# Kernel optimization log

Measured on AMD Instinct MI355X. Metric: run time of the kernel, lower is better.

## Reference

```python
import jax, jax.numpy as jnp
import numpy as np
import math

B, C, L, E, N = 16, 256, 2048, 512, 64
H = 2 * C  # S4 model dimension


def setup_inputs() -> dict:
    key = jax.random.key(0)
    ks = jax.random.split(key, 12)
    inp = {
        "x": jax.random.normal(ks[0], (B, C, L), dtype=jnp.float32),
        "diffusion_emb": jax.random.normal(ks[1], (B, E), dtype=jnp.float32),
        "dp_W": jax.random.normal(ks[2], (C, E), dtype=jnp.float32) / np.sqrt(E).astype(np.float32),
        "dp_b": jnp.zeros((C,), dtype=jnp.float32),
        "in_W": jax.random.normal(ks[3], (H, C), dtype=jnp.float32) / np.sqrt(C).astype(np.float32),
        "in_b": jnp.zeros((H,), dtype=jnp.float32),
        "out_W": jax.random.normal(ks[4], (2 * C, C), dtype=jnp.float32) / np.sqrt(C).astype(np.float32),
        "out_b": jnp.zeros((2 * C,), dtype=jnp.float32),
        "ln1_g": jnp.ones((H,), dtype=jnp.float32),
        "ln1_b": jnp.zeros((H,), dtype=jnp.float32),
        "ln2_g": jnp.ones((H,), dtype=jnp.float32),
        "ln2_b": jnp.zeros((H,), dtype=jnp.float32),
    }
    for i, pre in enumerate(["s41_", "s42_"]):
        k = jax.random.fold_in(key, 100 + i)
        k1, k2, k3, k4, k5 = jax.random.split(k, 5)
        # dt log-uniform in [1e-3, 1e-1] (standard S4 init)
        inp[pre + "log_dt"] = (jax.random.uniform(k1, (H,)) * (math.log(0.1) - math.log(0.001)) + math.log(0.001)).astype(jnp.float32)
        inp[pre + "A_re"] = (-0.5 * jnp.ones((H, N))).astype(jnp.float32)
        inp[pre + "A_im"] = jnp.tile(math.pi * jnp.arange(N, dtype=jnp.float32), (H, 1))
        inp[pre + "C_re"] = jax.random.normal(k2, (H, N), dtype=jnp.float32) * (0.5 ** 0.5)
        inp[pre + "C_im"] = jax.random.normal(k3, (H, N), dtype=jnp.float32) * (0.5 ** 0.5)
        inp[pre + "D"] = jax.random.normal(k4, (H,), dtype=jnp.float32)
        inp[pre + "oW"] = jax.random.normal(k5, (2 * H, H), dtype=jnp.float32) / np.sqrt(H).astype(np.float32)
        inp[pre + "ob"] = jnp.zeros((2 * H,), dtype=jnp.float32)
    return inp


def _s4(u, log_dt, A_re, A_im, C_re, C_im, D, oW, ob):
    # u: [B, H, L]. Diagonal SSM (S4D, ZOH discretization) -> FFT conv -> D skip -> GELU -> GLU output linear.
    Lq = u.shape[-1]
    dt = jnp.exp(log_dt)                       # [H]
    A = A_re + 1j * A_im                       # [H, N] diagonal state matrix
    Cc = C_re + 1j * C_im                      # [H, N]
    dtA = dt[:, None] * A                      # [H, N]
    Ct = Cc * (jnp.exp(dtA) - 1.0) / A         # ZOH-discretized C*B (B = 1)
    lr = jnp.arange(Lq)
    # Vandermonde kernel: K[h, l] = 2 Re sum_n Ct[h, n] exp(dtA[h, n] * l)
    K = 2.0 * jnp.real(jnp.einsum("hn,hnl->hl", Ct, jnp.exp(dtA[:, :, None] * lr)))  # [H, L]
    nfft = 2 * Lq
    y = jnp.fft.irfft(jnp.fft.rfft(u, n=nfft) * jnp.fft.rfft(K, n=nfft), n=nfft)[..., :Lq]
    y = y + D[None, :, None] * u
    y = jax.nn.gelu(y)
    y = jnp.einsum("oh,bhl->bol", oW, y) + ob[None, :, None]  # [B, 2H, L]
    a, b = jnp.split(y, 2, axis=1)             # GLU over channel dim
    return a * jax.nn.sigmoid(b)               # [B, H, L]


def _ln(y, g, b):
    # LayerNorm over the channel dim (module rearranges b c l -> b l c, LN(C), back)
    mu = jnp.mean(y, axis=1, keepdims=True)
    var = jnp.var(y, axis=1, keepdims=True)
    return (y - mu) * jax.lax.rsqrt(var + 1e-5) * g[None, :, None] + b[None, :, None]


def reference(x, diffusion_emb, dp_W, dp_b, in_W, in_b, out_W, out_b,
              ln1_g, ln1_b, ln2_g, ln2_b,
              s41_log_dt, s41_A_re, s41_A_im, s41_C_re, s41_C_im, s41_D, s41_oW, s41_ob,
              s42_log_dt, s42_A_re, s42_A_im, s42_C_re, s42_C_im, s42_D, s42_oW, s42_ob):
    d = diffusion_emb @ dp_W.T + dp_b          # [B, C] -> broadcast as [B, C, 1]
    y = x + d[:, :, None]
    y = jnp.einsum("oc,bcl->bol", in_W, y) + in_b[None, :, None]   # 1x1 conv: [B, 2C, L]
    y = _s4(y, s41_log_dt, s41_A_re, s41_A_im, s41_C_re, s41_C_im, s41_D, s41_oW, s41_ob)
    y = _ln(y, ln1_g, ln1_b)
    y = _s4(y, s42_log_dt, s42_A_re, s42_A_im, s42_C_re, s42_C_im, s42_D, s42_oW, s42_ob)
    y = _ln(y, ln2_g, ln2_b)
    gate, filt = jnp.split(y, 2, axis=1)
    y = jax.nn.sigmoid(gate) * jnp.tanh(filt)  # [B, C, L]
    y = jnp.einsum("oc,bcl->bol", out_W, y) + out_b[None, :, None]  # [B, 2C, L]
    residual, skip = jnp.split(y, 2, axis=1)
    return ((x + residual) / math.sqrt(2.0), skip)
```

## Files before the change

### kernel.cpp

```cpp
#include <hip/hip_runtime.h>
#include <math.h>

#define Bsz 16
#define Cch 256
#define Lsq 2048
#define Emb 512
#define Nst 64
#define Hch 512
#define KGP 2240

typedef _Float16 f16;
typedef _Float16 f16x8 __attribute__((ext_vector_type(8)));
typedef _Float16 f16x4 __attribute__((ext_vector_type(4)));
typedef float f32x4 __attribute__((ext_vector_type(4)));
typedef uint32_t u32x4 __attribute__((ext_vector_type(4)));

__device__ __forceinline__ float sigmoidf_(float x) { return 1.0f/(1.0f + __expf(-x)); }
__device__ __forceinline__ float gelu_tanh(float y) {
  float z = 0.7978845608028654f*(y + 0.044715f*y*y*y);
  return 0.5f*y*(1.0f + tanhf(z));
}

__device__ __forceinline__ void gload_lds16(const f16* g, f16* l) {
  __builtin_amdgcn_global_load_lds(
      (const __attribute__((address_space(1))) void*)g,
      (__attribute__((address_space(3))) void*)l, 16, 0, 0);
}


__global__ void k_emb(const float* __restrict__ emb, const float* __restrict__ dpW,
                      const float* __restrict__ dpb, float* __restrict__ d) {
  int b = blockIdx.x, c = threadIdx.x;
  const float* e = emb + b*Emb;
  const float* w = dpW + c*Emb;
  float s = dpb[c];
  for (int k = 0; k < Emb; ++k) s += e[k]*w[k];
  d[b*Cch + c] = s;
}

__global__ void k_f2h(const float* __restrict__ src, f16* __restrict__ dst, int n) {
  int i = blockIdx.x*256 + threadIdx.x;
  if (i < n) dst[i] = (f16)src[i];
}

__global__ void k_addemb(const float* __restrict__ x, const float* __restrict__ d,
                         f16* __restrict__ xd) {
  int i = blockIdx.x*256 + threadIdx.x;
  const float4* x4 = (const float4*)x;
  float4 v = x4[i];
  int bc = (i*4)/Lsq;
  float dd = d[bc];
  f16x4 o;
  o[0] = (f16)(v.x+dd); o[1] = (f16)(v.y+dd); o[2] = (f16)(v.z+dd); o[3] = (f16)(v.w+dd);
  ((f16x4*)xd)[i] = o;
}

__global__ void k_s4prep(const float* __restrict__ log_dt,
                         const float* __restrict__ A_re, const float* __restrict__ A_im,
                         const float* __restrict__ C_re, const float* __restrict__ C_im,
                         float* __restrict__ w_re, float* __restrict__ w_im,
                         float* __restrict__ ccr, float* __restrict__ cci) {
  int i = blockIdx.x*256 + threadIdx.x;
  if (i >= Hch*Nst) return;
  int h = i >> 6;
  float dt = expf(log_dt[h]);
  float Ar = A_re[i], Ai = A_im[i];
  float er = expf(dt*Ar);
  float wr = er*cosf(dt*Ai), wi = er*sinf(dt*Ai);
  float mag = Ar*Ar + Ai*Ai;
  float nr = wr - 1.0f, ni = wi;
  float qr = (nr*Ar + ni*Ai)/mag, qi = (ni*Ar - nr*Ai)/mag;
  float cr = C_re[i], ci = C_im[i];
  float tr = cr*qr - ci*qi, ti = cr*qi + ci*qr;
  w_re[i] = wr; w_im[i] = wi; ccr[i] = 2.0f*tr; cci[i] = -2.0f*ti;
}

__global__ __launch_bounds__(256) void k_kgen(
    const float* __restrict__ w_re, const float* __restrict__ w_im,
    const float* __restrict__ ccr, const float* __restrict__ cci,
    const float* __restrict__ Dvec,
    f16* __restrict__ Ke, f16* __restrict__ Ko) {
  __shared__ float2 wbt[64][65];
  __shared__ float2 wat[32][66];
  __shared__ float2 ccs[64];
  __shared__ float Kf[2048];
  int h = blockIdx.x, tid = threadIdx.x;
  if (tid < 64) {
    int n = tid;
    double wr = (double)w_re[h*64+n], wi = (double)w_im[h*64+n];
    double br = 1.0, bi = 0.0;
    for (int j = 0; j < 64; ++j) {
      wbt[n][j] = make_float2((float)br, (float)bi);
      double t = br*wr - bi*wi; bi = br*wi + bi*wr; br = t;
    }
    double ar = 1.0, ai = 0.0;
    for (int a = 0; a < 32; ++a) {
      wat[a][n] = make_float2((float)ar, (float)ai);
      double t = ar*br - ai*bi; ai = ar*bi + ai*br; ar = t;
    }
    ccs[n] = make_float2(ccr[h*64+n], cci[h*64+n]);
  }
  __syncthreads();
  int lane = tid & 63, wv = tid >> 6;
  float acc[8] = {0.f,0.f,0.f,0.f,0.f,0.f,0.f,0.f};
  for (int n = 0; n < 64; ++n) {
    float2 wb = wbt[n][lane];
    float2 cc = ccs[n];
    float tr = fmaf(cc.y, wb.y,  cc.x*wb.x);
    float ti = fmaf(cc.y, wb.x, -cc.x*wb.y);
    #pragma unroll
    for (int li = 0; li < 8; ++li) {
      float2 wa = wat[wv + 4*li][n];
      acc[li] = fmaf(wa.x, tr, acc[li]);
      acc[li] = fmaf(wa.y, ti, acc[li]);
    }
  }
  #pragma unroll
  for (int li = 0; li < 8; ++li)
    Kf[(wv + 4*li)*64 + lane] = acc[li];
  __syncthreads();
  if (tid == 0) Kf[0] += Dvec[h];
  __syncthreads();
  f16* keh = Ke + (size_t)h*KGP;
  f16* koh = Ko + (size_t)h*KGP;
  for (int q = tid; q < KGP; q += 256) {
    float e = (q < 2048) ? Kf[2047 - q] : 0.f;
    float o = (q < 2047) ? Kf[2046 - q] : 0.f;
    keh[q] = (f16)e; koh[q] = (f16)o;
  }
}

__device__ __forceinline__ f16x8 ldfrag(const f16* __restrict__ ke,
                                        const f16* __restrict__ ko, int q) {
  const f16* p = (q & 1) ? (ko + (q - 1)) : (ke + q);
  union { uint32_t u[4]; f16x8 v; } r;
  const uint32_t* pu = (const uint32_t*)p;
  r.u[0] = pu[0]; r.u[1] = pu[1]; r.u[2] = pu[2]; r.u[3] = pu[3];
  return r.v;
}

__global__ __launch_bounds__(256) void k_conv(
    const f16* __restrict__ u, const f16* __restrict__ Ke, const f16* __restrict__ Ko,
    f16* __restrict__ g) {
  __shared__ __align__(16) f16 Ul[16*2048];
  int h = blockIdx.x, tid = threadIdx.x;
  {
    int b = tid >> 4, pr = tid & 15;
    const f16* src = u + ((size_t)b*Hch + h)*Lsq;
    f16* dst = &Ul[b*2048];
    #pragma unroll
    for (int c = 0; c < 16; ++c) {
      int gs = c*16 + pr;
      *(f16x8*)&dst[(gs ^ b)*8] = *(const f16x8*)(src + gs*8);
    }
  }
  __syncthreads();
  int wv = tid >> 6, lane = tid & 63;
  int m = lane & 15, qd = lane >> 4;
  const f16* keh = Ke + (size_t)h*KGP;
  const f16* koh = Ko + (size_t)h*KGP;
  f16* gb = g + ((size_t)m*Hch + h)*Lsq;
  const f16* ulb = &Ul[m*2048];
  for (int pass = 0; pass < 4; ++pass) {
    int P = pass*4 + ((wv + pass) & 3);
    int i0 = P*128;
    int qb0 = 2047 - i0 - m + qd*8;
    f32x4 acc[8];
    #pragma unroll
    for (int t = 0; t < 8; ++t) acc[t] = (f32x4){0.f,0.f,0.f,0.f};
    f16x8 W[8];
    #pragma unroll
    for (int t = 0; t < 8; ++t) W[t] = ldfrag(keh, koh, qb0 - 16*t);
    int steps = 4*(P+1);
    for (int s4i = 0; s4i < steps; s4i += 4) {
      #pragma unroll
      for (int ph = 0; ph < 4; ++ph) {
        int s = s4i + ph;
        f16x8 bf = *(const f16x8*)&ulb[((4*s + qd) ^ m)*8];
        f16x8 nf0 = ldfrag(keh, koh, qb0 + 32*(s+1));
        f16x8 nf1 = ldfrag(keh, koh, qb0 - 16 + 32*(s+1));
        #pragma unroll
        for (int t = 0; t < 8; ++t)
          acc[t] = __builtin_amdgcn_mfma_f32_16x16x32_f16(W[(t - 2*ph) & 7], bf, acc[t], 0, 0, 0);
        W[(6 - 2*ph) & 7] = nf0;
        W[(7 - 2*ph) & 7] = nf1;
      }
    }
    #pragma unroll
    for (int t = 0; t < 8; ++t) {
      f16x4 o;
      #pragma unroll
      for (int r = 0; r < 4; ++r) o[r] = (f16)gelu_tanh(acc[t][r]);
      *(f16x4*)&gb[i0 + 16*t + qd*4] = o;
    }
  }
}

template<int KD, int MODE>
__global__ __launch_bounds__(256) void k_gemm(
    const f16* __restrict__ W, const f16* __restrict__ Bact,
    const float* __restrict__ bias, const float* __restrict__ xres,
    float* __restrict__ outF, f16* __restrict__ outH) {
  constexpr int TOFF = (MODE == 1) ? 512 : 256;
  __shared__ __align__(16) f16 As[2*128*64];
  __shared__ __align__(16) uint32_t Bs[32*132];
  int tid = threadIdx.x;
  int wv = tid >> 6, lane = tid & 63;
  int nt = blockIdx.x;
  int mt = blockIdx.y;
  int bb = nt >> 4;
  int l0 = (nt & 15)*128;
  int m0 = mt*128;
  int wm = (wv & 1)*64, wn = (wv >> 1)*64;
  int qd = lane >> 4, ln16 = lane & 15;

  f32x4 acc[2][4][4];
  #pragma unroll
  for (int t = 0; t < 2; ++t)
    for (int i = 0; i < 4; ++i)
      for (int j = 0; j < 4; ++j)
        acc[t][i][j] = (f32x4){0.f,0.f,0.f,0.f};

  const f16* Bbase = Bact + (size_t)bb*KD*Lsq + l0;
  int q16 = tid >> 4, nch = tid & 15;

  for (int kk = 0; kk < KD; kk += 64) {
    #pragma unroll
    for (int i = 0; i < 8; ++i) {
      int gbase = (wv*8 + i)*64;
      int G = gbase + lane;
      int t = G >> 10;
      int row = (G >> 3) & 127;
      int gsw = (G & 7) ^ (row & 7);
      const f16* src = W + (size_t)(m0 + row + t*TOFF)*KD + kk + gsw*8;
      gload_lds16(src, &As[gbase*8]);
    }
    #pragma unroll
    for (int c = 0; c < 2; ++c) {
      const f16* b0 = Bbase + (size_t)(kk + 2*q16 + 32*c)*Lsq + nch*8;
      f16x8 r0 = *(const f16x8*)b0;
      f16x8 r1 = *(const f16x8*)(b0 + Lsq);
      union { uint32_t w[8]; u32x4 v[2]; } pk;
      #pragma unroll
      for (int e = 0; e < 8; ++e) {
        union { f16 h2[2]; uint32_t u; } t2;
        t2.h2[0] = r0[e]; t2.h2[1] = r1[e];
        pk.w[e] = t2.u;
      }
      *(u32x4*)&Bs[(q16 + 16*c)*132 + nch*8]     = pk.v[0];
      *(u32x4*)&Bs[(q16 + 16*c)*132 + nch*8 + 4] = pk.v[1];
    }
    __syncthreads();
    #pragma unroll
    for (int s = 0; s < 2; ++s) {
      f16x8 afr[2][4];
      #pragma unroll
      for (int i = 0; i < 4; ++i)
        for (int t = 0; t < 2; ++t) {
          int row = wm + i*16 + ln16;
          int gp = (s*4 + qd) ^ (ln16 & 7);
          afr[t][i] = *(const f16x8*)&As[((t*128 + row)*8 + gp)*8];
        }
      f16x8 bfr[4];
      int bw0 = (s*16 + qd*4)*132 + wn + ln16;
      #pragma unroll
      for (int j = 0; j < 4; ++j) {
        union { uint32_t w2[4]; f16x8 v; } bu;
        #pragma unroll
        for (int r2 = 0; r2 < 4; ++r2) bu.w2[r2] = Bs[bw0 + j*16 + r2*132];
        bfr[j] = bu.v;
      }
      #pragma unroll
      for (int j = 0; j < 4; ++j)
        for (int i = 0; i < 4; ++i)
          for (int t = 0; t < 2; ++t)
            acc[t][i][j] = __builtin_amdgcn_mfma_f32_16x16x32_f16(afr[t][i], bfr[j], acc[t][i][j], 0, 0, 0);
    }
    __syncthreads();
  }

  #pragma unroll
  for (int i = 0; i < 4; ++i)
    for (int j = 0; j < 4; ++j)
      for (int r = 0; r < 4; ++r) {
        int ml = wm + i*16 + qd*4 + r;
        int nl = wn + j*16 + ln16;
        int mg = m0 + ml;
        int l  = l0 + nl;
        if (MODE == 0) {
          outH[((size_t)bb*Hch + mg)*Lsq + l]       = (f16)(acc[0][i][j][r] + bias[mg]);
          outH[((size_t)bb*Hch + mg + 256)*Lsq + l] = (f16)(acc[1][i][j][r] + bias[mg + 256]);
        } else if (MODE == 1) {
          float va = acc[0][i][j][r] + bias[mg];
          float vb = acc[1][i][j][r] + bias[512 + mg];
          outH[((size_t)bb*Hch + mg)*Lsq + l] = (f16)(va * sigmoidf_(vb));
        } else {
          size_t idx = ((size_t)bb*Cch + mg)*Lsq + l;
          float v0 = acc[0][i][j][r] + bias[mg];
          outF[idx] = (v0 + xres[idx]) * 0.7071067811865476f;
          float v1 = acc[1][i][j][r] + bias[mg + 256];
          outF[(size_t)Bsz*Cch*Lsq + idx] = v1;
        }
      }
}

template<int MODE>
__global__ __launch_bounds__(256) void k_ln(const f16* __restrict__ v,
                                            const float* __restrict__ gam, const float* __restrict__ bet,
                                            float* __restrict__ outF, f16* __restrict__ outH) {
  __shared__ float red[2][4][64];
  int b = blockIdx.x >> 5;
  int l = (blockIdx.x & 31)*64 + (threadIdx.x & 63);
  int wv = threadIdx.x >> 6, lane = threadIdx.x & 63;
  const f16* base = v + (size_t)b*Hch*Lsq + l;
  float s = 0.f, s2 = 0.f;
  for (int h = wv*128; h < wv*128 + 128; ++h) {
    float xv = (float)base[(size_t)h*Lsq];
    s += xv; s2 += xv*xv;
  }
  red[0][wv][lane] = s; red[1][wv][lane] = s2;
  __syncthreads();
  s  = red[0][0][lane] + red[0][1][lane] + red[0][2][lane] + red[0][3][lane];
  s2 = red[1][0][lane] + red[1][1][lane] + red[1][2][lane] + red[1][3][lane];
  float mu = s*(1.0f/Hch);
  float var = s2*(1.0f/Hch) - mu*mu;
  float rs = rsqrtf(var + 1e-5f);
  if (MODE == 0) {
    f16* ob = outH + (size_t)b*Hch*Lsq + l;
    for (int h = wv*128; h < wv*128 + 128; ++h)
      ob[(size_t)h*Lsq] = (f16)(((float)base[(size_t)h*Lsq] - mu)*rs*gam[h] + bet[h]);
  } else {
    f16* ob = outH + (size_t)b*Cch*Lsq + l;
    for (int c = wv*64; c < wv*64 + 64; ++c) {
      float xg = ((float)base[(size_t)c*Lsq] - mu)*rs*gam[c] + bet[c];
      float xf = ((float)base[(size_t)(c+Cch)*Lsq] - mu)*rs*gam[c+Cch] + bet[c+Cch];
      float xfc = fminf(fmaxf(xf, -15.f), 15.f);
      float e = __expf(2.f*xfc);
      ob[(size_t)c*Lsq] = (f16)(sigmoidf_(xg) * ((e-1.f)/(e+1.f)));
    }
  }
}

extern "C" void kernel_launch(void* const* d_in, const int* in_sizes, int n_in,
                              void* d_out, int out_size, void* d_ws, size_t ws_size,
                              hipStream_t stream) {
  const float* x    = (const float*)d_in[0];
  const float* emb  = (const float*)d_in[1];
  const float* dpW  = (const float*)d_in[2];
  const float* dpb  = (const float*)d_in[3];
  const float* inW  = (const float*)d_in[4];
  const float* inb  = (const float*)d_in[5];
  const float* outW = (const float*)d_in[6];
  const float* outb = (const float*)d_in[7];
  const float* ln1g = (const float*)d_in[8];
  const float* ln1b = (const float*)d_in[9];
  const float* ln2g = (const float*)d_in[10];
  const float* ln2b = (const float*)d_in[11];
  const float* s4[2][8];
  for (int ly = 0; ly < 2; ++ly)
    for (int k = 0; k < 8; ++k) s4[ly][k] = (const float*)d_in[12 + ly*8 + k];

  char* p = (char*)d_ws;
  auto alloc = [&](size_t bytes) { char* r = p; p += (bytes + 255) & ~(size_t)255; return r; };
  f16* inW16  = (f16*)alloc((size_t)Hch*Cch*2);
  f16* oW16_0 = (f16*)alloc((size_t)2*Hch*Hch*2);
  f16* oW16_1 = (f16*)alloc((size_t)2*Hch*Hch*2);
  f16* outW16 = (f16*)alloc((size_t)2*Cch*Cch*2);
  float* dbuf = (float*)alloc((size_t)Bsz*Cch*4);
  float* prm[2][4];
  for (int ly = 0; ly < 2; ++ly)
    for (int k = 0; k < 4; ++k) prm[ly][k] = (float*)alloc((size_t)Hch*Nst*4);
  f16* kge[2], *kgo[2];
  for (int ly = 0; ly < 2; ++ly) {
    kge[ly] = (f16*)alloc((size_t)Hch*KGP*2);
    kgo[ly] = (f16*)alloc((size_t)Hch*KGP*2);
  }
  f16*  xd   = (f16*)alloc((size_t)Bsz*Cch*Lsq*2);
  f16*  u16g = (f16*)alloc((size_t)Bsz*Hch*Lsq*2);
  f16*  gbuf = (f16*)alloc((size_t)Bsz*Hch*Lsq*2);
  f16*  glu  = (f16*)alloc((size_t)Bsz*Hch*Lsq*2);
  f16*  oW16[2] = {oW16_0, oW16_1};

  k_emb<<<Bsz, Cch, 0, stream>>>(emb, dpW, dpb, dbuf);
  k_f2h<<<(Hch*Cch+255)/256, 256, 0, stream>>>(inW, inW16, Hch*Cch);
  k_f2h<<<(2*Hch*Hch+255)/256, 256, 0, stream>>>(s4[0][6], oW16_0, 2*Hch*Hch);
  k_f2h<<<(2*Hch*Hch+255)/256, 256, 0, stream>>>(s4[1][6], oW16_1, 2*Hch*Hch);
  k_f2h<<<(2*Cch*Cch+255)/256, 256, 0, stream>>>(outW, outW16, 2*Cch*Cch);
  for (int ly = 0; ly < 2; ++ly) {
    k_s4prep<<<(Hch*Nst+255)/256, 256, 0, stream>>>(s4[ly][0], s4[ly][1], s4[ly][2],
        s4[ly][3], s4[ly][4], prm[ly][0], prm[ly][1], prm[ly][2], prm[ly][3]);
    k_kgen<<<Hch, 256, 0, stream>>>(prm[ly][0], prm[ly][1], prm[ly][2], prm[ly][3],
        s4[ly][5], kge[ly], kgo[ly]);
  }
  k_addemb<<<(Bsz*Cch*Lsq/4)/256, 256, 0, stream>>>(x, dbuf, xd);

  dim3 gg4(256, 4), gg2(256, 2), bl(256);
  k_gemm<Cch, 0><<<gg2, bl, 0, stream>>>(inW16, xd, inb, nullptr, nullptr, u16g);
  k_conv<<<Hch, 256, 0, stream>>>(u16g, kge[0], kgo[0], gbuf);
  k_gemm<Hch, 1><<<gg4, bl, 0, stream>>>(oW16[0], gbuf, s4[0][7], nullptr, nullptr, glu);
  k_ln<0><<<Bsz*32, 256, 0, stream>>>(glu, ln1g, ln1b, nullptr, u16g);
  k_conv<<<Hch, 256, 0, stream>>>(u16g, kge[1], kgo[1], gbuf);
  k_gemm<Hch, 1><<<gg4, bl, 0, stream>>>(oW16[1], gbuf, s4[1][7], nullptr, nullptr, glu);
  k_ln<1><<<Bsz*32, 256, 0, stream>>>(glu, ln2g, ln2b, nullptr, xd);
  k_gemm<Cch, 2><<<gg2, bl, 0, stream>>>(outW16, xd, outb, x, (float*)d_out, nullptr);
}
```

Baseline: 570.7 us.

## Double-buffer GEMM LDS tiles with K-step 32 to overlap loads and MFMA

Switches the 1x1-conv/GLU GEMM kernel from a single-buffered K=64 loop with two syncs per step to a double-buffered K=32 pipeline. The next A tile is issued via global_load_lds into the alternate buffer and B is prefetched into registers before the current MFMAs run, so only one barrier per step remains. The aim is to hide global memory latency behind compute. The cost is half the work per iteration, a changed swizzle, and extra registers for the prefetched B fragments.

```diff
diff --git a/kernel.cpp b/kernel.cpp
--- a/kernel.cpp
+++ b/kernel.cpp
@@ -202,8 +202,9 @@
     const float* __restrict__ bias, const float* __restrict__ xres,
     float* __restrict__ outF, f16* __restrict__ outH) {
   constexpr int TOFF = (MODE == 1) ? 512 : 256;
-  __shared__ __align__(16) f16 As[2*128*64];
-  __shared__ __align__(16) uint32_t Bs[32*132];
+  constexpr int NK = KD/32;
+  __shared__ __align__(16) f16 As[2][2*128*32];
+  __shared__ __align__(16) uint32_t Bs[2][16*132];
   int tid = threadIdx.x;
   int wv = tid >> 6, lane = tid & 63;
   int nt = blockIdx.x;
@@ -224,59 +225,74 @@
   const f16* Bbase = Bact + (size_t)bb*KD*Lsq + l0;
   int q16 = tid >> 4, nch = tid & 15;
 
-  for (int kk = 0; kk < KD; kk += 64) {
-    #pragma unroll
-    for (int i = 0; i < 8; ++i) {
-      int gbase = (wv*8 + i)*64;
+  auto stageA = [&](int buf, int kk) {
+    #pragma unroll
+    for (int i = 0; i < 4; ++i) {
+      int gbase = (wv*4 + i)*64;
       int G = gbase + lane;
-      int t = G >> 10;
-      int row = (G >> 3) & 127;
-      int gsw = (G & 7) ^ (row & 7);
+      int t = G >> 9;
+      int row = (G >> 2) & 127;
+      int gsw = (G & 3) ^ (row & 3);
       const f16* src = W + (size_t)(m0 + row + t*TOFF)*KD + kk + gsw*8;
-      gload_lds16(src, &As[gbase*8]);
-    }
-    #pragma unroll
-    for (int c = 0; c < 2; ++c) {
-      const f16* b0 = Bbase + (size_t)(kk + 2*q16 + 32*c)*Lsq + nch*8;
-      f16x8 r0 = *(const f16x8*)b0;
-      f16x8 r1 = *(const f16x8*)(b0 + Lsq);
-      union { uint32_t w[8]; u32x4 v[2]; } pk;
+      gload_lds16(src, &As[buf][gbase*8]);
+    }
+  };
+  f16x8 rb0, rb1;
+  auto loadB = [&](int kk) {
+    const f16* b0 = Bbase + (size_t)(kk + 2*q16)*Lsq + nch*8;
+    rb0 = *(const f16x8*)b0;
+    rb1 = *(const f16x8*)(b0 + Lsq);
+  };
+  auto packB = [&](int buf) {
+    union { uint32_t w[8]; u32x4 v[2]; } pk;
+    #pragma unroll
+    for (int e = 0; e < 8; ++e) {
+      union { f16 h2[2]; uint32_t u; } t2;
+      t2.h2[0] = rb0[e]; t2.h2[1] = rb1[e];
+      pk.w[e] = t2.u;
+    }
+    *(u32x4*)&Bs[buf][q16*132 + nch*8]     = pk.v[0];
+    *(u32x4*)&Bs[buf][q16*132 + nch*8 + 4] = pk.v[1];
+  };
+  auto compute = [&](int buf) {
+    f16x8 afr[2][4];
+    #pragma unroll
+    for (int i = 0; i < 4; ++i)
+      for (int t = 0; t < 2; ++t) {
+        int row = wm + i*16 + ln16;
+        int gp = qd ^ (ln16 & 3);
+        afr[t][i] = *(const f16x8*)&As[buf][((t*128 + row)*4 + gp)*8];
+      }
+    f16x8 bfr[4];
+    #pragma unroll
+    for (int j = 0; j < 4; ++j) {
+      union { uint32_t w2[4]; f16x8 v; } bu;
       #pragma unroll
-      for (int e = 0; e < 8; ++e) {
-        union { f16 h2[2]; uint32_t u; } t2;
-        t2.h2[0] = r0[e]; t2.h2[1] = r1[e];
-        pk.w[e] = t2.u;
-      }
-      *(u32x4*)&Bs[(q16 + 16*c)*132 + nch*8]     = pk.v[0];
-      *(u32x4*)&Bs[(q16 + 16*c)*132 + nch*8 + 4] = pk.v[1];
-    }
+      for (int r2 = 0; r2 < 4; ++r2) bu.w2[r2] = Bs[buf][(qd*4 + r2)*132 + wn + j*16 + ln16];
+      bfr[j] = bu.v;
+    }
+    #pragma unroll
+    for (int j = 0; j < 4; ++j)
+      for (int i = 0; i < 4; ++i)
+        for (int t = 0; t < 2; ++t)
+          acc[t][i][j] = __builtin_amdgcn_mfma_f32_16x16x32_f16(afr[t][i], bfr[j], acc[t][i][j], 0, 0, 0);
+  };
+
+  stageA(0, 0);
+  loadB(0);
+  packB(0);
+  __syncthreads();
+
+  int cur = 0;
+  for (int t = 0; t < NK; ++t) {
+    if (t + 1 < NK) {
+      stageA(cur ^ 1, (t + 1)*32);
+      loadB((t + 1)*32);
+    }
+    compute(cur);
+    if (t + 1 < NK) packB(cur ^ 1);
     __syncthreads();
-    #pragma unroll
-    for (int s = 0; s < 2; ++s) {
-      f16x8 afr[2][4];
-      #pragma unroll
-      for (int i = 0; i < 4; ++i)
-        for (int t = 0; t < 2; ++t) {
-          int row = wm + i*16 + ln16;
-          int gp = (s*4 + qd) ^ (ln16 & 7);
-          afr[t][i] = *(const f16x8*)&As[((t*128 + row)*8 + gp)*8];
-        }
-      f16x8 bfr[4];
-      int bw0 = (s*16 + qd*4)*132 + wn + ln16;
-      #pragma unroll
-      for (int j = 0; j < 4; ++j) {
-        union { uint32_t w2[4]; f16x8 v; } bu;
-        #pragma unroll
-        for (int r2 = 0; r2 < 4; ++r2) bu.w2[r2] = Bs[bw0 + j*16 + r2*132];
-        bfr[j] = bu.v;
-      }
-      #pragma unroll
-      for (int j = 0; j < 4; ++j)
-        for (int i = 0; i < 4; ++i)
-          for (int t = 0; t < 2; ++t)
-            acc[t][i][j] = __builtin_amdgcn_mfma_f32_16x16x32_f16(afr[t][i], bfr[j], acc[t][i][j], 0, 0, 0);
-    }
-    __syncthreads();
+    cur ^= 1;
   }
 
   #pragma unroll
```

Result: faster. 533.3 us (-6.5%).
